# Performance work log

Hardware: AMD Instinct MI355X
Metric: run time of the kernel (lower is better)

Reference implementation:

```python
import jax, jax.numpy as jnp
import numpy as np

B, L, D, H = 4, 2048, 1024, 16
DH = D // H


def setup_inputs() -> dict:
    key = jax.random.key(0)
    ks = jax.random.split(key, 8)
    scale = 1.0 / np.sqrt(D)
    q = jax.random.normal(ks[0], (B, L, D), dtype=jnp.float32)
    k = jax.random.normal(ks[1], (B, L, D), dtype=jnp.float32)
    v = jax.random.normal(ks[2], (B, L, D), dtype=jnp.float32)
    # causal mask: 1 = attend, 0 = masked (masked_fill(mask == 0, -inf))
    mask = jnp.tril(jnp.ones((L, L), dtype=bool))[None, None, :, :]
    mask = jnp.broadcast_to(mask, (B, 1, L, L))
    W_q = jax.random.normal(ks[3], (D, D), dtype=jnp.float32) * scale
    W_k = jax.random.normal(ks[4], (D, D), dtype=jnp.float32) * scale
    W_v = jax.random.normal(ks[5], (D, D), dtype=jnp.float32) * scale
    W_o = jax.random.normal(ks[6], (D, D), dtype=jnp.float32) * scale
    return {"q": q, "k": k, "v": v, "mask": mask,
            "W_q": W_q, "W_k": W_k, "W_v": W_v, "W_o": W_o}


def _split_heads(x):
    # [B, L, D] -> [B, H, L, DH]
    Bx, Lx, _ = x.shape
    return x.reshape(Bx, Lx, H, DH).transpose(0, 2, 1, 3)


def reference(q, k, v, mask, W_q, W_k, W_v, W_o):
    qh = _split_heads(q @ W_q.T)   # [B, H, L, DH]
    kh = _split_heads(k @ W_k.T)
    vh = _split_heads(v @ W_v.T)
    scores = jnp.einsum('bhqd,bhkd->bhqk', qh, kh) / np.sqrt(DH)
    scores = jnp.where(mask, scores, -jnp.inf)  # mask==0 -> -inf
    probs = jax.nn.softmax(scores, axis=-1)
    attn = jnp.einsum('bhqk,bhkd->bhqd', probs, vh)  # [B, H, L, DH]
    out = attn.transpose(0, 2, 1, 3).reshape(B, L, D)
    return out @ W_o.T
```

## Files before the change

kernel.cpp:

```cpp
#include <hip/hip_runtime.h>

typedef __attribute__((ext_vector_type(4))) float  f32x4;
typedef __attribute__((ext_vector_type(8))) short  s16x8;
typedef __attribute__((ext_vector_type(8))) unsigned short u16x8;
typedef __attribute__((ext_vector_type(4))) unsigned short u16x4;

static __device__ __forceinline__ unsigned short f2bf(float f) {
    unsigned int u = __builtin_bit_cast(unsigned int, f);
    u += 0x7fffu + ((u >> 16) & 1u);
    return (unsigned short)(u >> 16);
}

static __device__ __forceinline__ unsigned int cvt_pk_bf16(float lo, float hi) {
    unsigned int r;
    asm("v_cvt_pk_bf16_f32 %0, %1, %2" : "=v"(r) : "v"(lo), "v"(hi));
    return r;
}

static __device__ __forceinline__ void gload16(const void* g, void* l) {
    __builtin_amdgcn_global_load_lds(
        (const __attribute__((address_space(1))) void*)g,
        (__attribute__((address_space(3))) void*)l, 16, 0, 0);
}

__global__ __launch_bounds__(256)
void conv_kernel(const float* __restrict__ q, const float* __restrict__ k,
                 const float* __restrict__ v,
                 const float* __restrict__ wq, const float* __restrict__ wk,
                 const float* __restrict__ wv, const float* __restrict__ wo,
                 unsigned short* __restrict__ qb, unsigned short* __restrict__ kb,
                 unsigned short* __restrict__ vb, unsigned short* __restrict__ wb)
{
    const int bid = blockIdx.x;
    const float* src; unsigned short* dst; int inner;
    if      (bid < 4096)  { src = q;  dst = qb; inner = bid; }
    else if (bid < 8192)  { src = k;  dst = kb; inner = bid - 4096; }
    else if (bid < 12288) { src = v;  dst = vb; inner = bid - 8192; }
    else {
        const int wseg = (bid - 12288) >> 9;
        src = wseg == 0 ? wq : wseg == 1 ? wk : wseg == 2 ? wv : wo;
        dst = wb + (size_t)wseg * 1048576;
        inner = (bid - 12288) & 511;
    }
    const size_t e0 = (size_t)inner * 2048 + threadIdx.x * 8;
    f32x4 a = *(const f32x4*)(src + e0);
    f32x4 b = *(const f32x4*)(src + e0 + 4);
    u16x8 o;
    #pragma unroll
    for (int i = 0; i < 4; ++i) { o[i] = f2bf(a[i]); o[i + 4] = f2bf(b[i]); }
    *(u16x8*)(dst + e0) = o;
}

template<int EPI>
__global__ __launch_bounds__(512)
void gemm3(const unsigned short* __restrict__ A0,
           const unsigned short* __restrict__ A1,
           const unsigned short* __restrict__ A2,
           const unsigned short* __restrict__ Bw,
           unsigned short* __restrict__ O0, unsigned short* __restrict__ O1,
           unsigned short* __restrict__ O2, float* __restrict__ Of)
{
    __shared__ unsigned short Asw[3][256 * 64];
    __shared__ unsigned short Bsw[3][128 * 64];

    const int tid  = threadIdx.x;
    const int lane = tid & 63;
    const int wave = tid >> 6;
    const int wr   = wave >> 1, wc = wave & 1;
    const int g    = lane >> 4, l16 = lane & 15;

    const int nblk = (EPI == 0) ? 768 : 256;
    const int cpx  = nblk >> 3;
    const int wg   = (blockIdx.x & 7) * cpx + (blockIdx.x >> 3);
    const int bx   = wg & 7;
    const int byt  = wg >> 3;
    const int seg  = (EPI == 0) ? (byt >> 5) : 0;
    const int byl  = (EPI == 0) ? (byt & 31) : byt;

    const unsigned short* Ap = (EPI == 0) ? (seg == 0 ? A0 : seg == 1 ? A1 : A2) : A0;
    const unsigned short* Arow = Ap + (size_t)(byl * 256) * 1024;
    const unsigned short* Brow = Bw + (size_t)seg * 1048576 + (size_t)(bx * 128) * 1024;

    f32x4 acc[4][4] = {};

    auto stage = [&](int buf, int kt) {
        #pragma unroll
        for (int j = 0; j < 4; ++j) {
            const int idx = j * 512 + tid;
            const int r   = idx >> 3;
            const int cl  = (tid & 7) ^ (r & 7);
            gload16(Arow + (size_t)r * 1024 + kt * 64 + cl * 8,
                    (char*)Asw[buf] + j * 8192 + wave * 1024);
        }
        #pragma unroll
        for (int j = 0; j < 2; ++j) {
            const int idx = j * 512 + tid;
            const int r   = idx >> 3;
            const int cl  = (tid & 7) ^ (r & 7);
            gload16(Brow + (size_t)r * 1024 + kt * 64 + cl * 8,
                    (char*)Bsw[buf] + j * 8192 + wave * 1024);
        }
    };

    stage(0, 0);
    stage(1, 1);
    asm volatile("s_waitcnt vmcnt(6)" ::: "memory");
    __builtin_amdgcn_s_barrier();

    for (int kt = 0; kt < 16; ++kt) {
        if (kt + 2 < 16) stage((kt + 2) % 3, kt + 2);

        const char* Ab = (const char*)Asw[kt % 3];
        const char* Bb = (const char*)Bsw[kt % 3];
        #pragma unroll
        for (int ks = 0; ks < 2; ++ks) {
            s16x8 af[4], bf[4];
            #pragma unroll
            for (int mi = 0; mi < 4; ++mi) {
                const int row = wr * 64 + mi * 16 + l16;
                const int off = (row * 128 + g * 16 + ks * 64) ^ ((row & 7) << 4);
                af[mi] = __builtin_bit_cast(s16x8, *(const u16x8*)(Ab + off));
            }
            #pragma unroll
            for (int ni = 0; ni < 4; ++ni) {
                const int row = wc * 64 + ni * 16 + l16;
                const int off = (row * 128 + g * 16 + ks * 64) ^ ((row & 7) << 4);
                bf[ni] = __builtin_bit_cast(s16x8, *(const u16x8*)(Bb + off));
            }
            __builtin_amdgcn_s_setprio(1);
            #pragma unroll
            for (int mi = 0; mi < 4; ++mi)
                #pragma unroll
                for (int ni = 0; ni < 4; ++ni)
                    acc[mi][ni] = __builtin_amdgcn_mfma_f32_16x16x32_bf16(
                        af[mi], bf[ni], acc[mi][ni], 0, 0, 0);
            __builtin_amdgcn_s_setprio(0);
        }

        if (kt + 2 < 16) asm volatile("s_waitcnt vmcnt(6)" ::: "memory");
        else             asm volatile("s_waitcnt vmcnt(0)" ::: "memory");
        __builtin_amdgcn_s_barrier();
    }

    #pragma unroll
    for (int mi = 0; mi < 4; ++mi) {
        #pragma unroll
        for (int ni = 0; ni < 4; ++ni) {
            const int gr0 = byl * 256 + wr * 64 + mi * 16 + g * 4;
            const int gc  = bx * 128 + wc * 64 + ni * 16 + l16;
            if (EPI == 0 && seg == 2) {
                const int b = gr0 >> 11, ll = gr0 & 2047;
                const int h = gc >> 6,  dh = gc & 63;
                u16x4 pk;
                #pragma unroll
                for (int rr = 0; rr < 4; ++rr) pk[rr] = f2bf(acc[mi][ni][rr]);
                *(u16x4*)(O2 + (size_t)((b * 16 + h) * 64 + dh) * 2048 + ll) = pk;
            } else {
                #pragma unroll
                for (int rr = 0; rr < 4; ++rr) {
                    const int gr = gr0 + rr;
                    float v = acc[mi][ni][rr];
                    if (EPI == 0) {
                        const int b = gr >> 11, ll = gr & 2047;
                        const int h = gc >> 6,  dh = gc & 63;
                        if (seg == 0) {
                            v *= 0.125f;
                            O0[(size_t)((b * 16 + h) * 2048 + ll) * 64 + dh] = f2bf(v);
                        } else {
                            O1[(size_t)((b * 16 + h) * 2048 + ll) * 64 + dh] = f2bf(v);
                        }
                    } else {
                        Of[(size_t)gr * 1024 + gc] = v;
                    }
                }
            }
        }
    }
}

template<int AM, int BM, int EPI>
__global__ __launch_bounds__(256)
void gemm_k(const void* __restrict__ A0, const void* __restrict__ A1,
            const void* __restrict__ A2,
            const void* __restrict__ B0, const void* __restrict__ B1,
            const void* __restrict__ B2,
            unsigned short* __restrict__ O0, unsigned short* __restrict__ O1,
            unsigned short* __restrict__ O2, float* __restrict__ Of)
{
    __shared__ unsigned short Asw[128 * 64];
    __shared__ unsigned short Bsw[128 * 64];

    const int tid  = threadIdx.x;
    const int lane = tid & 63;
    const int wave = tid >> 6;
    const int wr   = wave >> 1, wc = wave & 1;
    const int g    = lane >> 4, l16 = lane & 15;

    const int nper = (EPI == 0) ? 192 : 64;
    const int wg   = (blockIdx.x & 7) * nper + (blockIdx.x >> 3);
    const int bx   = wg & 7;
    const int by   = wg >> 3;
    const int seg  = (EPI == 0) ? (by >> 6) : 0;
    const int byl  = (EPI == 0) ? (by & 63) : by;

    const void* Ap = seg == 0 ? A0 : seg == 1 ? A1 : A2;
    const void* Bp = seg == 0 ? B0 : seg == 1 ? B1 : B2;

    f32x4 acc[4][4] = {};

    for (int kt = 0; kt < 16; ++kt) {
        __syncthreads();
        if (AM == 0) {
            #pragma unroll
            for (int j = 0; j < 4; ++j) {
                const int idx = j * 256 + tid;
                const int r   = idx >> 3;
                const int cl  = (tid & 7) ^ (r & 7);
                gload16((const unsigned short*)Ap + (size_t)(byl * 128 + r) * 1024 + kt * 64 + cl * 8,
                        (char*)Asw + j * 4096 + wave * 1024);
            }
        } else {
            #pragma unroll
            for (int j = 0; j < 4; ++j) {
                const int idx = j * 256 + tid;
                const int r = idx >> 3, c = tid & 7;
                const float* src = (const float*)Ap + (size_t)(byl * 128 + r) * 1024 + kt * 64 + c * 8;
                f32x4 a = *(const f32x4*)src;
                f32x4 b = *(const f32x4*)(src + 4);
                u16x8 w;
                #pragma unroll
                for (int i = 0; i < 4; ++i) { w[i] = f2bf(a[i]); w[i + 4] = f2bf(b[i]); }
                *(u16x8*)((char*)Asw + ((r * 128 + c * 16) ^ ((r & 7) << 4))) = w;
            }
        }
        if (BM == 0) {
            #pragma unroll
            for (int j = 0; j < 4; ++j) {
                const int idx = j * 256 + tid;
                const int r   = idx >> 3;
                const int cl  = (tid & 7) ^ (r & 7);
                gload16((const unsigned short*)Bp + (size_t)(bx * 128 + r) * 1024 + kt * 64 + cl * 8,
                        (char*)Bsw + j * 4096 + wave * 1024);
            }
        } else {
            #pragma unroll
            for (int j = 0; j < 4; ++j) {
                const int idx = j * 256 + tid;
                const int r = idx >> 3, c = tid & 7;
                const float* src = (const float*)Bp + (size_t)(bx * 128 + r) * 1024 + kt * 64 + c * 8;
                f32x4 a = *(const f32x4*)src;
                f32x4 b = *(const f32x4*)(src + 4);
                u16x8 w;
                #pragma unroll
                for (int i = 0; i < 4; ++i) { w[i] = f2bf(a[i]); w[i + 4] = f2bf(b[i]); }
                *(u16x8*)((char*)Bsw + ((r * 128 + c * 16) ^ ((r & 7) << 4))) = w;
            }
        }
        __syncthreads();

        #pragma unroll
        for (int ks = 0; ks < 2; ++ks) {
            s16x8 af[4], bf[4];
            #pragma unroll
            for (int mi = 0; mi < 4; ++mi) {
                const int row = wr * 64 + mi * 16 + l16;
                const int off = (row * 128 + g * 16 + ks * 64) ^ ((row & 7) << 4);
                af[mi] = __builtin_bit_cast(s16x8, *(const u16x8*)((const char*)Asw + off));
            }
            #pragma unroll
            for (int ni = 0; ni < 4; ++ni) {
                const int row = wc * 64 + ni * 16 + l16;
                const int off = (row * 128 + g * 16 + ks * 64) ^ ((row & 7) << 4);
                bf[ni] = __builtin_bit_cast(s16x8, *(const u16x8*)((const char*)Bsw + off));
            }
            #pragma unroll
            for (int mi = 0; mi < 4; ++mi)
                #pragma unroll
                for (int ni = 0; ni < 4; ++ni)
                    acc[mi][ni] = __builtin_amdgcn_mfma_f32_16x16x32_bf16(
                        af[mi], bf[ni], acc[mi][ni], 0, 0, 0);
        }
    }

    #pragma unroll
    for (int mi = 0; mi < 4; ++mi) {
        #pragma unroll
        for (int ni = 0; ni < 4; ++ni) {
            #pragma unroll
            for (int rr = 0; rr < 4; ++rr) {
                const int gr = byl * 128 + wr * 64 + mi * 16 + g * 4 + rr;
                const int gc = bx * 128 + wc * 64 + ni * 16 + l16;
                float v = acc[mi][ni][rr];
                if (EPI == 0) {
                    const int b = gr >> 11, ll = gr & 2047, h = gc >> 6, dh = gc & 63;
                    if (seg == 0) {
                        v *= 0.125f;
                        O0[(size_t)((b * 16 + h) * 2048 + ll) * 64 + dh] = f2bf(v);
                    } else if (seg == 1) {
                        O1[(size_t)((b * 16 + h) * 2048 + ll) * 64 + dh] = f2bf(v);
                    } else {
                        O2[(size_t)((b * 16 + h) * 64 + dh) * 2048 + ll] = f2bf(v);
                    }
                } else {
                    Of[(size_t)gr * 1024 + gc] = v;
                }
            }
        }
    }
}

__global__ __launch_bounds__(512)
void attn_kernel(const unsigned short* __restrict__ Qh,
                 const unsigned short* __restrict__ Kh,
                 const unsigned short* __restrict__ Vt,
                 unsigned short* __restrict__ Ctx)
{
    __shared__ unsigned short Ksw[2][64 * 64];
    __shared__ unsigned short Vsw[2][64 * 64];
    __shared__ unsigned short Psw[8][16 * 64];

    const int tid  = threadIdx.x;
    const int lane = tid & 63;
    const int wave = tid >> 6;
    const int g    = lane >> 4, l16 = lane & 15;
    const int qb   = 15 - (int)(blockIdx.x >> 6);
    const int bh   = blockIdx.x & 63;
    const int b    = bh >> 4, h = bh & 15;
    const int qrow0 = qb * 128 + wave * 16;
    const int ntile = 2 * qb + 2;

    const int sr = tid >> 3, sc = tid & 7;
    const int soff = (sr * 128 + sc * 16) ^ ((sr & 7) << 4);
    const unsigned short* kbase = Kh + ((size_t)bh * 2048 + sr) * 64 + sc * 8;
    const unsigned short* vbase = Vt + ((size_t)bh * 64 + sr) * 2048 + sc * 8;

    s16x8 qf[2];
    {
        const unsigned short* qp = Qh + ((size_t)bh * 2048 + qrow0 + l16) * 64 + g * 8;
        qf[0] = __builtin_bit_cast(s16x8, *(const u16x8*)qp);
        qf[1] = __builtin_bit_cast(s16x8, *(const u16x8*)(qp + 32));
    }

    f32x4 o[4] = {};
    float m = -3.0e38f, l = 0.f;

    *(u16x8*)((char*)Ksw[0] + soff) = *(const u16x8*)kbase;
    *(u16x8*)((char*)Vsw[0] + soff) = *(const u16x8*)vbase;
    __syncthreads();

    int cur = 0;
    for (int t = 0; t < ntile; ++t) {
        const int kv0 = t * 64;

        u16x8 kn, vn;
        const bool hn = (t + 1 < ntile);
        if (hn) {
            kn = *(const u16x8*)(kbase + (size_t)(kv0 + 64) * 64);
            vn = *(const u16x8*)(vbase + (kv0 + 64));
        }

        if (kv0 <= qrow0 + 15) {
            const char* Kb = (const char*)Ksw[cur];
            const char* Vb = (const char*)Vsw[cur];

            f32x4 st[4] = {};
            __builtin_amdgcn_s_setprio(1);
            #pragma unroll
            for (int nt = 0; nt < 4; ++nt) {
                #pragma unroll
                for (int ks = 0; ks < 2; ++ks) {
                    const int row = nt * 16 + l16;
                    const int off = (row * 128 + g * 16 + ks * 64) ^ ((row & 7) << 4);
                    s16x8 kf = __builtin_bit_cast(s16x8, *(const u16x8*)(Kb + off));
                    st[nt] = __builtin_amdgcn_mfma_f32_16x16x32_bf16(kf, qf[ks], st[nt], 0, 0, 0);
                }
            }
            __builtin_amdgcn_s_setprio(0);

            if (kv0 + 63 > qrow0) {
                const int q_g = qrow0 + l16;
                #pragma unroll
                for (int nt = 0; nt < 4; ++nt)
                    #pragma unroll
                    for (int rr = 0; rr < 4; ++rr) {
                        const int kv_g = kv0 + nt * 16 + g * 4 + rr;
                        if (kv_g > q_g) st[nt][rr] = -3.0e38f;
                    }
            }

            float pmax = fmaxf(
                fmaxf(fmaxf(fmaxf(st[0][0], st[0][1]), fmaxf(st[0][2], st[0][3])),
                      fmaxf(fmaxf(st[1][0], st[1][1]), fmaxf(st[1][2], st[1][3]))),
                fmaxf(fmaxf(fmaxf(st[2][0], st[2][1]), fmaxf(st[2][2], st[2][3])),
                      fmaxf(fmaxf(st[3][0], st[3][1]), fmaxf(st[3][2], st[3][3]))));
            pmax = fmaxf(pmax, __shfl_xor(pmax, 16));
            pmax = fmaxf(pmax, __shfl_xor(pmax, 32));

            if (__all(pmax <= m + 8.0f)) {
                float r0 = 0.f;
                #pragma unroll
                for (int nt = 0; nt < 4; ++nt)
                    #pragma unroll
                    for (int rr = 0; rr < 4; ++rr) {
                        const float p = __expf(st[nt][rr] - m);
                        st[nt][rr] = p;
                        r0 += p;
                    }
                r0 += __shfl_xor(r0, 16);
                r0 += __shfl_xor(r0, 32);
                l += r0;
            } else {
                const float mn = fmaxf(m, pmax);
                const float scf = __expf(m - mn);
                m = mn;
                float r0 = 0.f;
                #pragma unroll
                for (int nt = 0; nt < 4; ++nt)
                    #pragma unroll
                    for (int rr = 0; rr < 4; ++rr) {
                        const float p = __expf(st[nt][rr] - mn);
                        st[nt][rr] = p;
                        r0 += p;
                    }
                r0 += __shfl_xor(r0, 16);
                r0 += __shfl_xor(r0, 32);
                l = l * scf + r0;
                float sc4[4];
                #pragma unroll
                for (int rr = 0; rr < 4; ++rr) sc4[rr] = __shfl(scf, g * 4 + rr);
                #pragma unroll
                for (int nt = 0; nt < 4; ++nt)
                    #pragma unroll
                    for (int rr = 0; rr < 4; ++rr)
                        o[nt][rr] *= sc4[rr];
            }

            unsigned short* Pw = Psw[wave];
            #pragma unroll
            for (int nt = 0; nt < 4; ++nt) {
                const unsigned int w0 = cvt_pk_bf16(st[nt][0], st[nt][1]);
                const unsigned int w1 = cvt_pk_bf16(st[nt][2], st[nt][3]);
                const int off = (l16 * 128 + nt * 32 + g * 8) ^ ((l16 & 7) << 4);
                const unsigned long long dw = ((unsigned long long)w1 << 32) | w0;
                *(unsigned long long*)((char*)Pw + off) = dw;
            }

            __builtin_amdgcn_s_setprio(1);
            #pragma unroll
            for (int ks = 0; ks < 2; ++ks) {
                const int offp = (l16 * 128 + g * 16 + ks * 64) ^ ((l16 & 7) << 4);
                s16x8 pf = __builtin_bit_cast(s16x8, *(const u16x8*)((const char*)Pw + offp));
                #pragma unroll
                for (int nt = 0; nt < 4; ++nt) {
                    const int row = nt * 16 + l16;
                    const int off = (row * 128 + g * 16 + ks * 64) ^ ((row & 7) << 4);
                    s16x8 vf = __builtin_bit_cast(s16x8, *(const u16x8*)(Vb + off));
                    o[nt] = __builtin_amdgcn_mfma_f32_16x16x32_bf16(pf, vf, o[nt], 0, 0, 0);
                }
            }
            __builtin_amdgcn_s_setprio(0);
        }

        if (hn) {
            *(u16x8*)((char*)Ksw[cur ^ 1] + soff) = kn;
            *(u16x8*)((char*)Vsw[cur ^ 1] + soff) = vn;
        }
        __syncthreads();
        cur ^= 1;
    }

    #pragma unroll
    for (int rr = 0; rr < 4; ++rr) {
        const float lq = __shfl(l, g * 4 + rr);
        const float inv = 1.0f / lq;
        const int q_g = qrow0 + g * 4 + rr;
        #pragma unroll
        for (int nt = 0; nt < 4; ++nt) {
            const int d = nt * 16 + l16;
            Ctx[((size_t)b * 2048 + q_g) * 1024 + h * 64 + d] = f2bf(o[nt][rr] * inv);
        }
    }
}

extern "C" void kernel_launch(void* const* d_in, const int* in_sizes, int n_in,
                              void* d_out, int out_size, void* d_ws, size_t ws_size,
                              hipStream_t stream)
{
    const float* q  = (const float*)d_in[0];
    const float* k  = (const float*)d_in[1];
    const float* v  = (const float*)d_in[2];
    const float* Wq = (const float*)d_in[4];
    const float* Wk = (const float*)d_in[5];
    const float* Wv = (const float*)d_in[6];
    const float* Wo = (const float*)d_in[7];

    const size_t NE = (size_t)4 * 16 * 2048 * 64;
    const size_t WE = (size_t)1024 * 1024;
    unsigned short* Qh = (unsigned short*)d_ws;
    unsigned short* Kh = Qh + NE;
    unsigned short* Vt = Kh + NE;
    float* outp = (float*)d_out;
    dim3 blk(256);

    if (ws_size >= 6 * NE * 2 + 4 * WE * 2) {
        unsigned short* qb  = Vt + NE;
        unsigned short* kb  = qb + NE;
        unsigned short* vb  = kb + NE;
        unsigned short* wb  = vb + NE;
        unsigned short* Ctx = qb;
        conv_kernel<<<dim3(14336), blk, 0, stream>>>(q, k, v, Wq, Wk, Wv, Wo,
                                                     qb, kb, vb, wb);
        gemm3<0><<<dim3(768), dim3(512), 0, stream>>>(
            qb, kb, vb, wb, Qh, Kh, Vt, nullptr);
        attn_kernel<<<dim3(1024), dim3(512), 0, stream>>>(Qh, Kh, Vt, Ctx);
        gemm3<1><<<dim3(256), dim3(512), 0, stream>>>(
            Ctx, nullptr, nullptr, wb + 3 * WE, nullptr, nullptr, nullptr, outp);
    } else {
        unsigned short* Ctx = Vt + NE;
        gemm_k<1, 1, 0><<<dim3(1536), blk, 0, stream>>>(
            q, k, v, Wq, Wk, Wv, Qh, Kh, Vt, nullptr);
        attn_kernel<<<dim3(1024), dim3(512), 0, stream>>>(Qh, Kh, Vt, Ctx);
        gemm_k<0, 1, 1><<<dim3(512), blk, 0, stream>>>(
            Ctx, nullptr, nullptr, Wo, nullptr, nullptr,
            nullptr, nullptr, nullptr, outp);
    }
}
```

Before: 192.8 us.

## Interleave GEMM global prefetch and LDS reads into four barrier-separated MFMA phases

The projection GEMM main loop is restructured from one bulk prefetch followed by two MFMA k-steps into four phases. Each phase issues a slice of LDS fragment loads and part of the next tile's global-to-LDS prefetch, then runs eight MFMAs under raised priority. Scheduling barriers and workgroup barriers pin the order. The aim is to spread memory traffic across the compute and overlap it better with MFMA work, in the style of ping-pong scheduled kernels. The cost is several extra s_barrier calls per k-tile and stricter lgkmcnt waits that could stall waves.

```diff
diff --git a/kernel.cpp b/kernel.cpp
--- a/kernel.cpp
+++ b/kernel.cpp
@@ -53,7 +53,7 @@
 
 template<int EPI>
 __global__ __launch_bounds__(512)
-void gemm3(const unsigned short* __restrict__ A0,
+void gemm8(const unsigned short* __restrict__ A0,
            const unsigned short* __restrict__ A1,
            const unsigned short* __restrict__ A2,
            const unsigned short* __restrict__ Bw,
@@ -83,62 +83,128 @@
 
     f32x4 acc[4][4] = {};
 
-    auto stage = [&](int buf, int kt) {
-        #pragma unroll
-        for (int j = 0; j < 4; ++j) {
-            const int idx = j * 512 + tid;
-            const int r   = idx >> 3;
-            const int cl  = (tid & 7) ^ (r & 7);
-            gload16(Arow + (size_t)r * 1024 + kt * 64 + cl * 8,
-                    (char*)Asw[buf] + j * 8192 + wave * 1024);
-        }
-        #pragma unroll
-        for (int j = 0; j < 2; ++j) {
-            const int idx = j * 512 + tid;
-            const int r   = idx >> 3;
-            const int cl  = (tid & 7) ^ (r & 7);
-            gload16(Brow + (size_t)r * 1024 + kt * 64 + cl * 8,
-                    (char*)Bsw[buf] + j * 8192 + wave * 1024);
-        }
+    auto stageA = [&](int buf, int kt2, int j) {
+        const int idx = j * 512 + tid;
+        const int r   = idx >> 3;
+        const int cl  = (tid & 7) ^ (r & 7);
+        gload16(Arow + (size_t)r * 1024 + kt2 * 64 + cl * 8,
+                (char*)Asw[buf] + j * 8192 + wave * 1024);
     };
-
-    stage(0, 0);
-    stage(1, 1);
+    auto stageB = [&](int buf, int kt2, int j) {
+        const int idx = j * 512 + tid;
+        const int r   = idx >> 3;
+        const int cl  = (tid & 7) ^ (r & 7);
+        gload16(Brow + (size_t)r * 1024 + kt2 * 64 + cl * 8,
+                (char*)Bsw[buf] + j * 8192 + wave * 1024);
+    };
+    auto lda = [&](const char* Ab, int mi, int ks) -> s16x8 {
+        const int row = wr * 64 + mi * 16 + l16;
+        const int off = (row * 128 + g * 16 + ks * 64) ^ ((row & 7) << 4);
+        return __builtin_bit_cast(s16x8, *(const u16x8*)(Ab + off));
+    };
+    auto ldb = [&](const char* Bb, int ni, int ks) -> s16x8 {
+        const int row = wc * 64 + ni * 16 + l16;
+        const int off = (row * 128 + g * 16 + ks * 64) ^ ((row & 7) << 4);
+        return __builtin_bit_cast(s16x8, *(const u16x8*)(Bb + off));
+    };
+
+    #pragma unroll
+    for (int j = 0; j < 4; ++j) stageA(0, 0, j);
+    #pragma unroll
+    for (int j = 0; j < 2; ++j) stageB(0, 0, j);
+    #pragma unroll
+    for (int j = 0; j < 4; ++j) stageA(1, 1, j);
+    #pragma unroll
+    for (int j = 0; j < 2; ++j) stageB(1, 1, j);
     asm volatile("s_waitcnt vmcnt(6)" ::: "memory");
     __builtin_amdgcn_s_barrier();
 
     for (int kt = 0; kt < 16; ++kt) {
-        if (kt + 2 < 16) stage((kt + 2) % 3, kt + 2);
-
         const char* Ab = (const char*)Asw[kt % 3];
         const char* Bb = (const char*)Bsw[kt % 3];
-        #pragma unroll
-        for (int ks = 0; ks < 2; ++ks) {
-            s16x8 af[4], bf[4];
-            #pragma unroll
-            for (int mi = 0; mi < 4; ++mi) {
-                const int row = wr * 64 + mi * 16 + l16;
-                const int off = (row * 128 + g * 16 + ks * 64) ^ ((row & 7) << 4);
-                af[mi] = __builtin_bit_cast(s16x8, *(const u16x8*)(Ab + off));
-            }
-            #pragma unroll
-            for (int ni = 0; ni < 4; ++ni) {
-                const int row = wc * 64 + ni * 16 + l16;
-                const int off = (row * 128 + g * 16 + ks * 64) ^ ((row & 7) << 4);
-                bf[ni] = __builtin_bit_cast(s16x8, *(const u16x8*)(Bb + off));
-            }
-            __builtin_amdgcn_s_setprio(1);
-            #pragma unroll
-            for (int mi = 0; mi < 4; ++mi)
-                #pragma unroll
-                for (int ni = 0; ni < 4; ++ni)
-                    acc[mi][ni] = __builtin_amdgcn_mfma_f32_16x16x32_bf16(
-                        af[mi], bf[ni], acc[mi][ni], 0, 0, 0);
-            __builtin_amdgcn_s_setprio(0);
-        }
-
-        if (kt + 2 < 16) asm volatile("s_waitcnt vmcnt(6)" ::: "memory");
-        else             asm volatile("s_waitcnt vmcnt(0)" ::: "memory");
+        const bool st  = (kt + 2 < 16);
+        const int  sb  = (kt + 2) % 3;
+        const int  kn  = kt + 2;
+        s16x8 a0, a1, a2, a3, b0, b1, b2, b3;
+
+        b0 = ldb(Bb, 0, 0); b1 = ldb(Bb, 1, 0); b2 = ldb(Bb, 2, 0); b3 = ldb(Bb, 3, 0);
+        a0 = lda(Ab, 0, 0); a1 = lda(Ab, 1, 0);
+        if (st) { stageA(sb, kn, 0); stageA(sb, kn, 1); }
+        __builtin_amdgcn_sched_barrier(0);
+        __builtin_amdgcn_s_barrier();
+        asm volatile("s_waitcnt lgkmcnt(0)" ::: "memory");
+        __builtin_amdgcn_sched_barrier(0);
+        __builtin_amdgcn_s_setprio(1);
+        acc[0][0] = __builtin_amdgcn_mfma_f32_16x16x32_bf16(a0, b0, acc[0][0], 0, 0, 0);
+        acc[0][1] = __builtin_amdgcn_mfma_f32_16x16x32_bf16(a0, b1, acc[0][1], 0, 0, 0);
+        acc[0][2] = __builtin_amdgcn_mfma_f32_16x16x32_bf16(a0, b2, acc[0][2], 0, 0, 0);
+        acc[0][3] = __builtin_amdgcn_mfma_f32_16x16x32_bf16(a0, b3, acc[0][3], 0, 0, 0);
+        acc[1][0] = __builtin_amdgcn_mfma_f32_16x16x32_bf16(a1, b0, acc[1][0], 0, 0, 0);
+        acc[1][1] = __builtin_amdgcn_mfma_f32_16x16x32_bf16(a1, b1, acc[1][1], 0, 0, 0);
+        acc[1][2] = __builtin_amdgcn_mfma_f32_16x16x32_bf16(a1, b2, acc[1][2], 0, 0, 0);
+        acc[1][3] = __builtin_amdgcn_mfma_f32_16x16x32_bf16(a1, b3, acc[1][3], 0, 0, 0);
+        __builtin_amdgcn_s_setprio(0);
+        __builtin_amdgcn_sched_barrier(0);
+        __builtin_amdgcn_s_barrier();
+
+        a2 = lda(Ab, 2, 0); a3 = lda(Ab, 3, 0);
+        if (st) { stageA(sb, kn, 2); stageA(sb, kn, 3); }
+        __builtin_amdgcn_sched_barrier(0);
+        __builtin_amdgcn_s_barrier();
+        asm volatile("s_waitcnt lgkmcnt(0)" ::: "memory");
+        __builtin_amdgcn_sched_barrier(0);
+        __builtin_amdgcn_s_setprio(1);
+        acc[2][0] = __builtin_amdgcn_mfma_f32_16x16x32_bf16(a2, b0, acc[2][0], 0, 0, 0);
+        acc[2][1] = __builtin_amdgcn_mfma_f32_16x16x32_bf16(a2, b1, acc[2][1], 0, 0, 0);
+        acc[2][2] = __builtin_amdgcn_mfma_f32_16x16x32_bf16(a2, b2, acc[2][2], 0, 0, 0);
+        acc[2][3] = __builtin_amdgcn_mfma_f32_16x16x32_bf16(a2, b3, acc[2][3], 0, 0, 0);
+        acc[3][0] = __builtin_amdgcn_mfma_f32_16x16x32_bf16(a3, b0, acc[3][0], 0, 0, 0);
+        acc[3][1] = __builtin_amdgcn_mfma_f32_16x16x32_bf16(a3, b1, acc[3][1], 0, 0, 0);
+        acc[3][2] = __builtin_amdgcn_mfma_f32_16x16x32_bf16(a3, b2, acc[3][2], 0, 0, 0);
+        acc[3][3] = __builtin_amdgcn_mfma_f32_16x16x32_bf16(a3, b3, acc[3][3], 0, 0, 0);
+        __builtin_amdgcn_s_setprio(0);
+        __builtin_amdgcn_sched_barrier(0);
+        __builtin_amdgcn_s_barrier();
+
+        b0 = ldb(Bb, 0, 1); b1 = ldb(Bb, 1, 1); b2 = ldb(Bb, 2, 1); b3 = ldb(Bb, 3, 1);
+        a0 = lda(Ab, 0, 1); a1 = lda(Ab, 1, 1);
+        if (st) { stageB(sb, kn, 0); }
+        __builtin_amdgcn_sched_barrier(0);
+        __builtin_amdgcn_s_barrier();
+        asm volatile("s_waitcnt lgkmcnt(0)" ::: "memory");
+        __builtin_amdgcn_sched_barrier(0);
+        __builtin_amdgcn_s_setprio(1);
+        acc[0][0] = __builtin_amdgcn_mfma_f32_16x16x32_bf16(a0, b0, acc[0][0], 0, 0, 0);
+        acc[0][1] = __builtin_amdgcn_mfma_f32_16x16x32_bf16(a0, b1, acc[0][1], 0, 0, 0);
+        acc[0][2] = __builtin_amdgcn_mfma_f32_16x16x32_bf16(a0, b2, acc[0][2], 0, 0, 0);
+        acc[0][3] = __builtin_amdgcn_mfma_f32_16x16x32_bf16(a0, b3, acc[0][3], 0, 0, 0);
+        acc[1][0] = __builtin_amdgcn_mfma_f32_16x16x32_bf16(a1, b0, acc[1][0], 0, 0, 0);
+        acc[1][1] = __builtin_amdgcn_mfma_f32_16x16x32_bf16(a1, b1, acc[1][1], 0, 0, 0);
+        acc[1][2] = __builtin_amdgcn_mfma_f32_16x16x32_bf16(a1, b2, acc[1][2], 0, 0, 0);
+        acc[1][3] = __builtin_amdgcn_mfma_f32_16x16x32_bf16(a1, b3, acc[1][3], 0, 0, 0);
+        __builtin_amdgcn_s_setprio(0);
+        __builtin_amdgcn_sched_barrier(0);
+        __builtin_amdgcn_s_barrier();
+
+        a2 = lda(Ab, 2, 1); a3 = lda(Ab, 3, 1);
+        if (st) { stageB(sb, kn, 1); }
+        __builtin_amdgcn_sched_barrier(0);
+        __builtin_amdgcn_s_barrier();
+        asm volatile("s_waitcnt lgkmcnt(0)" ::: "memory");
+        __builtin_amdgcn_sched_barrier(0);
+        __builtin_amdgcn_s_setprio(1);
+        acc[2][0] = __builtin_amdgcn_mfma_f32_16x16x32_bf16(a2, b0, acc[2][0], 0, 0, 0);
+        acc[2][1] = __builtin_amdgcn_mfma_f32_16x16x32_bf16(a2, b1, acc[2][1], 0, 0, 0);
+        acc[2][2] = __builtin_amdgcn_mfma_f32_16x16x32_bf16(a2, b2, acc[2][2], 0, 0, 0);
+        acc[2][3] = __builtin_amdgcn_mfma_f32_16x16x32_bf16(a2, b3, acc[2][3], 0, 0, 0);
+        acc[3][0] = __builtin_amdgcn_mfma_f32_16x16x32_bf16(a3, b0, acc[3][0], 0, 0, 0);
+        acc[3][1] = __builtin_amdgcn_mfma_f32_16x16x32_bf16(a3, b1, acc[3][1], 0, 0, 0);
+        acc[3][2] = __builtin_amdgcn_mfma_f32_16x16x32_bf16(a3, b2, acc[3][2], 0, 0, 0);
+        acc[3][3] = __builtin_amdgcn_mfma_f32_16x16x32_bf16(a3, b3, acc[3][3], 0, 0, 0);
+        __builtin_amdgcn_s_setprio(0);
+        if (st)                asm volatile("s_waitcnt vmcnt(6)" ::: "memory");
+        else if (kt + 1 < 16)  asm volatile("s_waitcnt vmcnt(0)" ::: "memory");
+        __builtin_amdgcn_sched_barrier(0);
         __builtin_amdgcn_s_barrier();
     }
 
@@ -510,10 +576,10 @@
         unsigned short* Ctx = qb;
         conv_kernel<<<dim3(14336), blk, 0, stream>>>(q, k, v, Wq, Wk, Wv, Wo,
                                                      qb, kb, vb, wb);
-        gemm3<0><<<dim3(768), dim3(512), 0, stream>>>(
+        gemm8<0><<<dim3(768), dim3(512), 0, stream>>>(
             qb, kb, vb, wb, Qh, Kh, Vt, nullptr);
         attn_kernel<<<dim3(1024), dim3(512), 0, stream>>>(Qh, Kh, Vt, Ctx);
-        gemm3<1><<<dim3(256), dim3(512), 0, stream>>>(
+        gemm8<1><<<dim3(256), dim3(512), 0, stream>>>(
             Ctx, nullptr, nullptr, wb + 3 * WE, nullptr, nullptr, nullptr, outp);
     } else {
         unsigned short* Ctx = Vt + NE;
```

Result: no change. 196.5 us (+1.9%).
